# Optimization experiments

Measured on AMD Instinct MI355X. Metric: run time of the kernel, lower is better.

## Reference

```python
import jax, jax.numpy as jnp
import numpy as np

DIM = 192
H = W = 56
WS = 7
SS = 3
NH = 6
HIDDEN = int(DIM * 4.0)
B = 32


def layer_norm(x, g, b, eps=1e-5):
    mu = jnp.mean(x, axis=-1, keepdims=True)
    var = jnp.var(x, axis=-1, keepdims=True)
    return (x - mu) * jax.lax.rsqrt(var + eps) * g + b


def window_partition(x, ws):
    # x: [B, H, W, C] -> [B*nW, ws*ws, C]
    Bb, Hh, Ww, C = x.shape
    x = x.reshape(Bb, Hh // ws, ws, Ww // ws, ws, C)
    x = x.transpose(0, 1, 3, 2, 4, 5)
    return x.reshape(-1, ws * ws, C)


def window_reverse(win, ws, Hh, Ww):
    C = win.shape[-1]
    Bb = win.shape[0] // ((Hh // ws) * (Ww // ws))
    x = win.reshape(Bb, Hh // ws, Ww // ws, ws, ws, C)
    x = x.transpose(0, 1, 3, 2, 4, 5)
    return x.reshape(Bb, Hh, Ww, C)


def setup_inputs() -> dict:
    key = jax.random.key(0)
    ks = jax.random.split(key, 14)
    s = 0.02
    return {
        "x": jax.random.normal(ks[0], (B, H * W, DIM), jnp.float32),
        "qkv_w": jax.random.normal(ks[1], (DIM, 3 * DIM), jnp.float32) * s,
        "qkv_b": jnp.zeros((3 * DIM,), jnp.float32),
        "proj_w": jax.random.normal(ks[2], (DIM, DIM), jnp.float32) * s,
        "proj_b": jnp.zeros((DIM,), jnp.float32),
        "g1": jnp.ones((DIM,), jnp.float32),
        "be1": jnp.zeros((DIM,), jnp.float32),
        "g2": jnp.ones((DIM,), jnp.float32),
        "be2": jnp.zeros((DIM,), jnp.float32),
        "w1": jax.random.normal(ks[3], (DIM, HIDDEN), jnp.float32) * s,
        "b1": jnp.zeros((HIDDEN,), jnp.float32),
        "w2": jax.random.normal(ks[4], (HIDDEN, DIM), jnp.float32) * s,
        "b2": jnp.zeros((DIM,), jnp.float32),
    }


def reference(x, qkv_w, qkv_b, proj_w, proj_b, g1, be1, g2, be2, w1, b1, w2, b2):
    Bb, L, C = x.shape
    hd = C // NH
    scale = hd ** (-0.5)
    x4 = x.reshape(Bb, H, W, C)
    # cyclic shift
    shifted = jnp.roll(x4, shift=(-SS, -SS), axis=(1, 2))
    win = window_partition(shifted, WS)              # [B_, N, C]
    B_, N, _ = win.shape
    xn = layer_norm(win, g1, be1)
    qkv = xn @ qkv_w + qkv_b                          # [B_, N, 3C]
    qkv = qkv.reshape(B_, N, 3, NH, hd).transpose(2, 0, 3, 1, 4)
    q, k, v = qkv[0], qkv[1], qkv[2]                  # [B_, NH, N, hd]
    attn = jnp.einsum('bhnd,bhmd->bhnm', q, k) * scale
    attn = jax.nn.softmax(attn, axis=-1)
    out = jnp.einsum('bhnm,bhmd->bhnd', attn, v)
    out = out.transpose(0, 2, 1, 3).reshape(B_, N, C)
    out = out @ proj_w + proj_b
    x4 = window_reverse(out, WS, H, W)
    x4 = jnp.roll(x4, shift=(SS, SS), axis=(1, 2))
    x = x4.reshape(Bb, H * W, C)
    # MLP with residual
    xn2 = layer_norm(x, g2, be2)
    h = jax.nn.gelu(xn2 @ w1 + b1, approximate=False)
    return x + (h @ w2 + b2)
```

## Files before the change

kernel.cpp:

```cpp
#include <hip/hip_runtime.h>

typedef unsigned short u16;
typedef unsigned int   u32;
typedef __attribute__((ext_vector_type(8))) short bf16x8;
typedef __attribute__((ext_vector_type(4))) float f32x4;

#define DIMC   192
#define HH     56
#define WSZ    7
#define SSH    3
#define NTOK   49
#define NWIN_T 2048
#define HIDDEN 768
#define LTOT   3136

#define LDA    200
#define LDSS   68
#define LDPU   136
#define LDVT   72

#define OFF_QKV 0
#define OFF_PW  110592
#define OFF_W1  147456
#define OFF_W2  294912
#define WS_ELEMS 442368
#define WS_BYTES (WS_ELEMS * 2)
#define XATTN_BYTES ((size_t)NWIN_T * NTOK * DIMC * 2)

#define MFMA(a,b,c) __builtin_amdgcn_mfma_f32_16x16x32_bf16((a),(b),(c),0,0,0)

__device__ __forceinline__ float bf2f(u16 u) {
    union { u32 i; float f; } v; v.i = ((u32)u) << 16; return v.f;
}
__device__ __forceinline__ u16 f2bf(float f) {
    union { float ff; u32 i; } v; v.ff = f;
    u32 x = v.i;
    return (u16)((x + 0x7FFFu + ((x >> 16) & 1u)) >> 16);
}

__global__ void cvt_weights(const float* __restrict__ qkv_w,
                            const float* __restrict__ proj_w,
                            const float* __restrict__ w1,
                            const float* __restrict__ w2,
                            u16* __restrict__ ws)
{
    const int idx = blockIdx.x * blockDim.x + threadIdx.x;
    const int stride = gridDim.x * blockDim.x;
    for (int i = idx; i < 110592; i += stride) {
        int k = i / 576, n = i - k * 576;
        ws[OFF_QKV + n * 192 + k] = f2bf(qkv_w[i]);
    }
    for (int i = idx; i < 36864; i += stride) {
        int k = i / 192, n = i - k * 192;
        ws[OFF_PW + n * 192 + k] = f2bf(proj_w[i]);
    }
    for (int i = idx; i < 147456; i += stride) {
        int k = i / 768, n = i - k * 768;
        ws[OFF_W1 + n * 192 + k] = f2bf(w1[i]);
    }
    for (int i = idx; i < 147456; i += stride) {
        int k = i / 192, n = i - k * 192;
        ws[OFF_W2 + n * 768 + k] = f2bf(w2[i]);
    }
}

__device__ __forceinline__ void ln1_gather(
    const float* __restrict__ x, const float* __restrict__ g1,
    const float* __restrict__ be1, u16* __restrict__ s_A,
    int b, int wi, int wj, int wv, int lane)
{
    for (int t = wv; t < 64; t += 4) {
        if (t < NTOK) {
            const int pi = t / 7, pj = t - pi * 7;
            const int si = (wi * WSZ + pi + SSH) % HH;
            const int sj = (wj * WSZ + pj + SSH) % HH;
            const float* src = x + ((size_t)b * LTOT + si * HH + sj) * DIMC;
            float v0 = src[lane], v1 = src[lane + 64], v2 = src[lane + 128];
            float s  = v0 + v1 + v2;
            float s2 = v0 * v0 + v1 * v1 + v2 * v2;
#pragma unroll
            for (int off = 32; off > 0; off >>= 1) {
                s  += __shfl_xor(s,  off);
                s2 += __shfl_xor(s2, off);
            }
            const float mu   = s * (1.f / 192.f);
            const float rstd = rsqrtf(s2 * (1.f / 192.f) - mu * mu + 1e-5f);
            s_A[t*LDA + lane      ] = f2bf((v0-mu)*rstd*g1[lane]     + be1[lane]);
            s_A[t*LDA + lane + 64 ] = f2bf((v1-mu)*rstd*g1[lane+64]  + be1[lane+64]);
            s_A[t*LDA + lane + 128] = f2bf((v2-mu)*rstd*g1[lane+128] + be1[lane+128]);
        } else {
            s_A[t*LDA + lane] = 0; s_A[t*LDA + lane + 64] = 0; s_A[t*LDA + lane + 128] = 0;
        }
    }
}

__device__ __forceinline__ void attn_all(
    u16* __restrict__ s_A, u16* __restrict__ s_Q,
    float* __restrict__ Sf, u16* __restrict__ PU, u16* __restrict__ Vt,
    const u16* __restrict__ Wqkvt, const float* __restrict__ qkv_b,
    int tid, int wv, int ar, int ak, int rg0)
{
    const float scale = 0.1767766952966369f;
    f32x4 o[12];

    bf16x8 ax[4][6];
#pragma unroll
    for (int mt = 0; mt < 4; mt++)
#pragma unroll
        for (int kk = 0; kk < 6; kk++)
            ax[mt][kk] = *(const bf16x8*)&s_A[(mt*16 + ar)*LDA + kk*32 + ak];

#pragma unroll
    for (int G = 0; G < 3; G++) {
#pragma unroll
        for (int tl = 0; tl < 3; tl++) {
            const int tt = wv*3 + tl;
            const int section = tt >> 2, idxq = tt & 3;
            const int gcol = section*192 + G*64 + idxq*16 + ar;
            const int lcol = section*64 + idxq*16 + ar;
            const float bias = qkv_b[gcol];
            const u16* wc = Wqkvt + (size_t)gcol * 192;
            f32x4 acc[4];
#pragma unroll
            for (int mt = 0; mt < 4; mt++) acc[mt] = 0;
#pragma unroll
            for (int kk = 0; kk < 6; kk++) {
                bf16x8 bh = *(const bf16x8*)&wc[kk*32 + ak];
#pragma unroll
                for (int mt = 0; mt < 4; mt++)
                    acc[mt] = MFMA(ax[mt][kk], bh, acc[mt]);
            }
#pragma unroll
            for (int mt = 0; mt < 4; mt++)
#pragma unroll
                for (int rg = 0; rg < 4; rg++)
                    s_Q[(mt*16 + rg0 + rg)*LDA + lcol] = f2bf(acc[mt][rg] + bias);
        }
        __syncthreads();

#pragma unroll
        for (int HL = 0; HL < 2; HL++) {
            {
                bf16x8 bk = *(const bf16x8*)&s_Q[(wv*16 + ar)*LDA + 64 + HL*32 + ak];
#pragma unroll
                for (int mt = 0; mt < 4; mt++) {
                    bf16x8 aq = *(const bf16x8*)&s_Q[(mt*16 + ar)*LDA + HL*32 + ak];
                    f32x4 sa; sa = 0;
                    sa = MFMA(aq, bk, sa);
#pragma unroll
                    for (int rg = 0; rg < 4; rg++)
                        Sf[(mt*16 + rg0 + rg)*LDSS + wv*16 + ar] = sa[rg] * scale;
                }
            }
            __syncthreads();
            {
                const int row = tid >> 2, sub = tid & 3;
                if (row < NTOK) {
                    float e[16]; float m = -1e30f;
#pragma unroll
                    for (int i = 0; i < 16; i++) {
                        const int j = sub + 4*i;
                        e[i] = (j < NTOK) ? Sf[row*LDSS + j] : -1e30f;
                        m = fmaxf(m, e[i]);
                    }
                    m = fmaxf(m, __shfl_xor(m, 1));
                    m = fmaxf(m, __shfl_xor(m, 2));
                    float sum = 0.f;
#pragma unroll
                    for (int i = 0; i < 16; i++) { e[i] = __expf(e[i] - m); sum += e[i]; }
                    sum += __shfl_xor(sum, 1);
                    sum += __shfl_xor(sum, 2);
                    const float inv = 1.f / sum;
#pragma unroll
                    for (int i = 0; i < 16; i++) {
                        const int j = sub + 4*i;
                        const float p = e[i] * inv;
                        const u16 hb = f2bf(p);
                        PU[row*LDPU + j] = hb;
                        PU[row*LDPU + 64 + j] = f2bf(p - bf2f(hb));
                    }
                }
                for (int i2 = tid; i2 < 2048; i2 += 256) {
                    const int d = i2 & 31, j = i2 >> 5;
                    Vt[d*LDVT + j] = (j < NTOK) ? s_Q[j*LDA + 128 + HL*32 + d] : (u16)0;
                }
            }
            __syncthreads();
            {
                const int dcol = (wv & 1)*16 + ar;
                const int mtb = (wv >> 1) << 1;
#pragma unroll
                for (int mi = 0; mi < 2; mi++) {
                    f32x4 accv; accv = 0;
#pragma unroll
                    for (int kk = 0; kk < 2; kk++) {
                        bf16x8 ph = *(const bf16x8*)&PU[((mtb+mi)*16 + ar)*LDPU + kk*32 + ak];
                        bf16x8 pl = *(const bf16x8*)&PU[((mtb+mi)*16 + ar)*LDPU + 64 + kk*32 + ak];
                        bf16x8 bv = *(const bf16x8*)&Vt[dcol*LDVT + kk*32 + ak];
                        accv = MFMA(ph, bv, accv);
                        accv = MFMA(pl, bv, accv);
                    }
                    o[(G*2 + HL)*2 + mi] = accv;
                }
            }
            __syncthreads();
        }
    }

    {
        const int mtb = (wv >> 1) << 1;
        const int cbase = (wv & 1)*16 + ar;
#pragma unroll
        for (int hp = 0; hp < 6; hp++) {
            const int col = hp*32 + cbase;
#pragma unroll
            for (int mi = 0; mi < 2; mi++)
#pragma unroll
                for (int rg = 0; rg < 4; rg++)
                    s_A[((mtb+mi)*16 + rg0 + rg)*LDA + col] = f2bf(o[hp*2 + mi][rg]);
        }
    }
    __syncthreads();
}

__global__ __launch_bounds__(256, 2)
void swin_attn(const float* __restrict__ x,
               const float* __restrict__ qkv_b, const float* __restrict__ proj_b,
               const float* __restrict__ g1, const float* __restrict__ be1,
               const u16* __restrict__ wsw, u16* __restrict__ xattn)
{
    __shared__ __align__(16) u16 s_A[64 * LDA];
    __shared__ __align__(16) u16 s_Q[64 * LDA];
    __shared__ __align__(16) u16 s_R3[64 * LDPU + 32 * LDVT];

    float* const Sf = (float*)s_R3;
    u16*  const PU  = s_R3;
    u16*  const Vt  = s_R3 + 64 * LDPU;

    const int wid = blockIdx.x;
    const int b  = wid >> 6;
    const int wi = (wid >> 3) & 7;
    const int wj = wid & 7;
    const int tid  = threadIdx.x;
    const int wv   = tid >> 6;
    const int lane = tid & 63;
    const int ar   = lane & 15;
    const int ak   = (lane >> 4) << 3;
    const int rg0  = (lane >> 4) << 2;

    ln1_gather(x, g1, be1, s_A, b, wi, wj, wv, lane);
    __syncthreads();

    attn_all(s_A, s_Q, Sf, PU, Vt, wsw + OFF_QKV, qkv_b, tid, wv, ar, ak, rg0);

    {
        const u16* Wpt = wsw + OFF_PW;
        bf16x8 ao[4][6];
#pragma unroll
        for (int mt = 0; mt < 4; mt++)
#pragma unroll
            for (int kk = 0; kk < 6; kk++)
                ao[mt][kk] = *(const bf16x8*)&s_A[(mt*16 + ar)*LDA + kk*32 + ak];
#pragma unroll
        for (int ntl = 0; ntl < 3; ntl++) {
            const int col = (wv*3 + ntl)*16 + ar;
            const float bias = proj_b[col];
            const u16* wc = Wpt + (size_t)col * 192;
            f32x4 acc[4];
#pragma unroll
            for (int mt = 0; mt < 4; mt++) acc[mt] = 0;
#pragma unroll
            for (int kk = 0; kk < 6; kk++) {
                bf16x8 bh = *(const bf16x8*)&wc[kk*32 + ak];
#pragma unroll
                for (int mt = 0; mt < 4; mt++)
                    acc[mt] = MFMA(ao[mt][kk], bh, acc[mt]);
            }
#pragma unroll
            for (int mt = 0; mt < 4; mt++)
#pragma unroll
                for (int rg = 0; rg < 4; rg++) {
                    const int row = mt*16 + rg0 + rg;
                    if (row < NTOK)
                        xattn[((size_t)wid * NTOK + row) * DIMC + col] =
                            f2bf(acc[mt][rg] + bias);
                }
        }
    }
}

__global__ __launch_bounds__(256, 3)
void swin_mlp(const u16* __restrict__ xattn,
              const float* __restrict__ g2, const float* __restrict__ be2,
              const float* __restrict__ b1f, const float* __restrict__ b2f,
              const u16* __restrict__ wsw, float* __restrict__ out)
{
    __shared__ __align__(16) u16 s_X[64 * LDA];
    __shared__ __align__(16) u16 s_H[64 * LDA];

    const int tid  = threadIdx.x;
    const int wv   = tid >> 6;
    const int lane = tid & 63;
    const int ar   = lane & 15;
    const int ak   = (lane >> 4) << 3;
    const int rg0  = (lane >> 4) << 2;
    const int base = blockIdx.x * 64;
    const u16* W1t = wsw + OFF_W1;
    const u16* W2t = wsw + OFF_W2;

    for (int t = wv; t < 64; t += 4) {
        const u16* src = xattn + (size_t)(base + t) * DIMC;
        float v0 = bf2f(src[lane]);
        float v1 = bf2f(src[lane + 64]);
        float v2 = bf2f(src[lane + 128]);
        float s  = v0 + v1 + v2;
        float s2 = v0*v0 + v1*v1 + v2*v2;
#pragma unroll
        for (int off = 32; off > 0; off >>= 1) {
            s  += __shfl_xor(s,  off);
            s2 += __shfl_xor(s2, off);
        }
        const float mu   = s * (1.f / 192.f);
        const float rstd = rsqrtf(s2 * (1.f / 192.f) - mu * mu + 1e-5f);
        s_X[t*LDA + lane      ] = f2bf((v0-mu)*rstd*g2[lane]     + be2[lane]);
        s_X[t*LDA + lane + 64 ] = f2bf((v1-mu)*rstd*g2[lane+64]  + be2[lane+64]);
        s_X[t*LDA + lane + 128] = f2bf((v2-mu)*rstd*g2[lane+128] + be2[lane+128]);
    }
    __syncthreads();

    f32x4 accO[3][4];
#pragma unroll
    for (int i = 0; i < 3; i++)
#pragma unroll
        for (int m = 0; m < 4; m++) accO[i][m] = 0;

    for (int cc = 0; cc < 4; cc++) {
        {
            f32x4 acc1[3][4];
#pragma unroll
            for (int i = 0; i < 3; i++)
#pragma unroll
                for (int m = 0; m < 4; m++) acc1[i][m] = 0;
#pragma unroll
            for (int kk = 0; kk < 6; kk++) {
                bf16x8 a4[4];
#pragma unroll
                for (int mt = 0; mt < 4; mt++)
                    a4[mt] = *(const bf16x8*)&s_X[(mt*16 + ar)*LDA + kk*32 + ak];
#pragma unroll
                for (int ntl = 0; ntl < 3; ntl++) {
                    const int ngl = cc*192 + (wv*3 + ntl)*16 + ar;
                    bf16x8 w = *(const bf16x8*)&W1t[(size_t)ngl * 192 + kk*32 + ak];
#pragma unroll
                    for (int mt = 0; mt < 4; mt++)
                        acc1[ntl][mt] = MFMA(a4[mt], w, acc1[ntl][mt]);
                }
            }
#pragma unroll
            for (int ntl = 0; ntl < 3; ntl++) {
                const int ncol = (wv*3 + ntl)*16 + ar;
                const float bias = b1f[cc*192 + ncol];
#pragma unroll
                for (int mt = 0; mt < 4; mt++)
#pragma unroll
                    for (int rg = 0; rg < 4; rg++) {
                        const float z = acc1[ntl][mt][rg] + bias;
                        const float ge = 0.5f * z * (1.f + erff(z * 0.70710678118654752f));
                        s_H[(mt*16 + rg0 + rg)*LDA + ncol] = f2bf(ge);
                    }
            }
        }
        __syncthreads();
        {
#pragma unroll
            for (int kk = 0; kk < 6; kk++) {
                bf16x8 a4[4];
#pragma unroll
                for (int mt = 0; mt < 4; mt++)
                    a4[mt] = *(const bf16x8*)&s_H[(mt*16 + ar)*LDA + kk*32 + ak];
#pragma unroll
                for (int ntl = 0; ntl < 3; ntl++) {
                    const int col = (wv*3 + ntl)*16 + ar;
                    bf16x8 w = *(const bf16x8*)&W2t[(size_t)col * 768 + cc*192 + kk*32 + ak];
#pragma unroll
                    for (int mt = 0; mt < 4; mt++)
                        accO[ntl][mt] = MFMA(a4[mt], w, accO[ntl][mt]);
                }
            }
        }
        __syncthreads();
    }

#pragma unroll
    for (int ntl = 0; ntl < 3; ntl++) {
        const int col = (wv*3 + ntl)*16 + ar;
        const float bias = b2f[col];
#pragma unroll
        for (int mt = 0; mt < 4; mt++)
#pragma unroll
            for (int rg = 0; rg < 4; rg++) {
                const int grow = base + mt*16 + rg0 + rg;
                const int w = grow / 49, t = grow - w * 49;
                const int bb = w >> 6, wi = (w >> 3) & 7, wj = w & 7;
                const int pi = t / 7, pj = t - pi * 7;
                const int di = (wi * WSZ + pi + SSH) % HH;
                const int dj = (wj * WSZ + pj + SSH) % HH;
                out[((size_t)bb * LTOT + di * HH + dj) * DIMC + col] =
                    accO[ntl][mt][rg] + bias + bf2f(xattn[(size_t)grow * DIMC + col]);
            }
    }
}

__global__ __launch_bounds__(256, 2)
void swin_mono(const float* __restrict__ x,
               const float* __restrict__ qkv_b, const float* __restrict__ proj_b,
               const float* __restrict__ g1, const float* __restrict__ be1,
               const float* __restrict__ g2, const float* __restrict__ be2,
               const float* __restrict__ b1f, const float* __restrict__ b2f,
               const u16* __restrict__ wsw, float* __restrict__ out)
{
    __shared__ __align__(16) u16 s_A[64 * LDA];
    __shared__ __align__(16) u16 s_Q[64 * LDA];
    __shared__ __align__(16) u16 s_R3[64 * LDA];

    float* const Sf  = (float*)s_R3;
    u16*  const PU   = s_R3;
    u16*  const Vt   = s_R3 + 64 * LDPU;
    u16*  const s_H  = s_R3;
    u16*  const s_XW = s_Q;

    const int wid = blockIdx.x;
    const int b  = wid >> 6;
    const int wi = (wid >> 3) & 7;
    const int wj = wid & 7;
    const int tid  = threadIdx.x;
    const int wv   = tid >> 6;
    const int lane = tid & 63;
    const int ar   = lane & 15;
    const int ak   = (lane >> 4) << 3;
    const int rg0  = (lane >> 4) << 2;

    const u16* Wpt = wsw + OFF_PW;
    const u16* W1t = wsw + OFF_W1;
    const u16* W2t = wsw + OFF_W2;

    ln1_gather(x, g1, be1, s_A, b, wi, wj, wv, lane);
    __syncthreads();

    attn_all(s_A, s_Q, Sf, PU, Vt, wsw + OFF_QKV, qkv_b, tid, wv, ar, ak, rg0);

    {
        bf16x8 ao[4][6];
#pragma unroll
        for (int mt = 0; mt < 4; mt++)
#pragma unroll
            for (int kk = 0; kk < 6; kk++)
                ao[mt][kk] = *(const bf16x8*)&s_A[(mt*16 + ar)*LDA + kk*32 + ak];
#pragma unroll
        for (int ntl = 0; ntl < 3; ntl++) {
            const int col = (wv*3 + ntl)*16 + ar;
            const float bias = proj_b[col];
            const u16* wc = Wpt + (size_t)col * 192;
            f32x4 acc[4];
#pragma unroll
            for (int mt = 0; mt < 4; mt++) acc[mt] = 0;
#pragma unroll
            for (int kk = 0; kk < 6; kk++) {
                bf16x8 bh = *(const bf16x8*)&wc[kk*32 + ak];
#pragma unroll
                for (int mt = 0; mt < 4; mt++)
                    acc[mt] = MFMA(ao[mt][kk], bh, acc[mt]);
            }
#pragma unroll
            for (int mt = 0; mt < 4; mt++)
#pragma unroll
                for (int rg = 0; rg < 4; rg++)
                    s_XW[(mt*16 + rg0 + rg)*LDA + col] = f2bf(acc[mt][rg] + bias);
        }
    }
    __syncthreads();

    for (int t = wv; t < NTOK; t += 4) {
        float v0 = bf2f(s_XW[t*LDA + lane      ]);
        float v1 = bf2f(s_XW[t*LDA + lane + 64 ]);
        float v2 = bf2f(s_XW[t*LDA + lane + 128]);
        float s  = v0 + v1 + v2;
        float s2 = v0*v0 + v1*v1 + v2*v2;
#pragma unroll
        for (int off = 32; off > 0; off >>= 1) {
            s  += __shfl_xor(s,  off);
            s2 += __shfl_xor(s2, off);
        }
        const float mu   = s * (1.f / 192.f);
        const float rstd = rsqrtf(s2 * (1.f / 192.f) - mu * mu + 1e-5f);
        s_A[t*LDA + lane      ] = f2bf((v0-mu)*rstd*g2[lane]     + be2[lane]);
        s_A[t*LDA + lane + 64 ] = f2bf((v1-mu)*rstd*g2[lane+64]  + be2[lane+64]);
        s_A[t*LDA + lane + 128] = f2bf((v2-mu)*rstd*g2[lane+128] + be2[lane+128]);
    }
    __syncthreads();

    f32x4 accO[3][4];
#pragma unroll
    for (int i = 0; i < 3; i++)
#pragma unroll
        for (int m = 0; m < 4; m++) accO[i][m] = 0;

    for (int cc = 0; cc < 4; cc++) {
        {
            f32x4 acc1[3][4];
#pragma unroll
            for (int i = 0; i < 3; i++)
#pragma unroll
                for (int m = 0; m < 4; m++) acc1[i][m] = 0;
#pragma unroll
            for (int kk = 0; kk < 6; kk++) {
                bf16x8 a4[4];
#pragma unroll
                for (int mt = 0; mt < 4; mt++)
                    a4[mt] = *(const bf16x8*)&s_A[(mt*16 + ar)*LDA + kk*32 + ak];
#pragma unroll
                for (int ntl = 0; ntl < 3; ntl++) {
                    const int ngl = cc*192 + (wv*3 + ntl)*16 + ar;
                    bf16x8 w = *(const bf16x8*)&W1t[(size_t)ngl * 192 + kk*32 + ak];
#pragma unroll
                    for (int mt = 0; mt < 4; mt++)
                        acc1[ntl][mt] = MFMA(a4[mt], w, acc1[ntl][mt]);
                }
            }
#pragma unroll
            for (int ntl = 0; ntl < 3; ntl++) {
                const int ncol = (wv*3 + ntl)*16 + ar;
                const float bias = b1f[cc*192 + ncol];
#pragma unroll
                for (int mt = 0; mt < 4; mt++)
#pragma unroll
                    for (int rg = 0; rg < 4; rg++) {
                        const float z = acc1[ntl][mt][rg] + bias;
                        const float ge = 0.5f * z * (1.f + erff(z * 0.70710678118654752f));
                        s_H[(mt*16 + rg0 + rg)*LDA + ncol] = f2bf(ge);
                    }
            }
        }
        __syncthreads();
        {
#pragma unroll
            for (int kk = 0; kk < 6; kk++) {
                bf16x8 a4[4];
#pragma unroll
                for (int mt = 0; mt < 4; mt++)
                    a4[mt] = *(const bf16x8*)&s_H[(mt*16 + ar)*LDA + kk*32 + ak];
#pragma unroll
                for (int ntl = 0; ntl < 3; ntl++) {
                    const int col = (wv*3 + ntl)*16 + ar;
                    bf16x8 w = *(const bf16x8*)&W2t[(size_t)col * 768 + cc*192 + kk*32 + ak];
#pragma unroll
                    for (int mt = 0; mt < 4; mt++)
                        accO[ntl][mt] = MFMA(a4[mt], w, accO[ntl][mt]);
                }
            }
        }
        __syncthreads();
    }

#pragma unroll
    for (int ntl = 0; ntl < 3; ntl++) {
        const int col = (wv*3 + ntl)*16 + ar;
        const float bias = b2f[col];
#pragma unroll
        for (int mt = 0; mt < 4; mt++)
#pragma unroll
            for (int rg = 0; rg < 4; rg++) {
                const int row = mt*16 + rg0 + rg;
                if (row < NTOK) {
                    const int pi = row / 7, pj = row - pi * 7;
                    const int di = (wi * WSZ + pi + SSH) % HH;
                    const int dj = (wj * WSZ + pj + SSH) % HH;
                    out[((size_t)b * LTOT + di * HH + dj) * DIMC + col] =
                        accO[ntl][mt][rg] + bias + bf2f(s_XW[row*LDA + col]);
                }
            }
    }
}

extern "C" void kernel_launch(void* const* d_in, const int* in_sizes, int n_in,
                              void* d_out, int out_size, void* d_ws, size_t ws_size,
                              hipStream_t stream)
{
    const float* x      = (const float*)d_in[0];
    const float* qkv_w  = (const float*)d_in[1];
    const float* qkv_b  = (const float*)d_in[2];
    const float* proj_w = (const float*)d_in[3];
    const float* proj_b = (const float*)d_in[4];
    const float* g1     = (const float*)d_in[5];
    const float* be1    = (const float*)d_in[6];
    const float* g2     = (const float*)d_in[7];
    const float* be2    = (const float*)d_in[8];
    const float* w1     = (const float*)d_in[9];
    const float* b1     = (const float*)d_in[10];
    const float* w2     = (const float*)d_in[11];
    const float* b2     = (const float*)d_in[12];
    float* out = (float*)d_out;

    cvt_weights<<<256, 256, 0, stream>>>(qkv_w, proj_w, w1, w2, (u16*)d_ws);

    if (ws_size >= (size_t)WS_BYTES + XATTN_BYTES) {
        u16* xattn = (u16*)d_ws + WS_ELEMS;
        swin_attn<<<NWIN_T, 256, 0, stream>>>(x, qkv_b, proj_b, g1, be1,
                                              (const u16*)d_ws, xattn);
        swin_mlp<<<NTOK * NWIN_T / 64, 256, 0, stream>>>(xattn, g2, be2, b1, b2,
                                                         (const u16*)d_ws, out);
    } else {
        swin_mono<<<NWIN_T, 256, 0, stream>>>(x, qkv_b, proj_b, g1, be1, g2, be2,
                                              b1, b2, (const u16*)d_ws, out);
    }
}
```

Baseline: 349.8 us.

## Split fused MLP kernel into separate GEMM1+GELU and GEMM2+residual kernels

Replaces the single fused MLP kernel with two kernels: one does LayerNorm, the first GEMM and GELU over 64-row by 192-column chunks, writing the hidden activation to a bf16 workspace buffer. The second reads that buffer and performs the second GEMM, bias, residual and un-shift scatter. This gives four times more blocks for the first GEMM and lighter per-block register and LDS use, aiming at higher occupancy. In exchange it adds a large global round trip for the hidden tensor, recomputes LayerNorm per column chunk, and reads A operands for the second GEMM straight from global memory without LDS staging. The new path runs only if the workspace is large enough.

Result: slower. 451.7 us (+29.1%).

```diff
diff --git a/kernel.cpp b/kernel.cpp
--- a/kernel.cpp
+++ b/kernel.cpp
@@ -13,6 +13,7 @@
 #define NWIN_T 2048
 #define HIDDEN 768
 #define LTOT   3136
+#define NTOKENS 100352
 
 #define LDA    200
 #define LDSS   68
@@ -25,7 +26,10 @@
 #define OFF_W2  294912
 #define WS_ELEMS 442368
 #define WS_BYTES (WS_ELEMS * 2)
-#define XATTN_BYTES ((size_t)NWIN_T * NTOK * DIMC * 2)
+#define XATTN_ELEMS ((size_t)NWIN_T * NTOK * DIMC)
+#define XATTN_BYTES (XATTN_ELEMS * 2)
+#define H_ELEMS ((size_t)NTOKENS * HIDDEN)
+#define H_BYTES (H_ELEMS * 2)
 
 #define MFMA(a,b,c) __builtin_amdgcn_mfma_f32_16x16x32_bf16((a),(b),(c),0,0,0)
 
@@ -286,6 +290,138 @@
                             f2bf(acc[mt][rg] + bias);
                 }
         }
+    }
+}
+
+__global__ __launch_bounds__(256, 4)
+void mlp1_gelu(const u16* __restrict__ xattn,
+               const float* __restrict__ g2, const float* __restrict__ be2,
+               const float* __restrict__ b1f,
+               const u16* __restrict__ wsw, u16* __restrict__ hbuf)
+{
+    __shared__ __align__(16) u16 s_X[64 * LDA];
+
+    const int bid = blockIdx.x;
+    const int rb = bid >> 2, cchunk = bid & 3;
+    const size_t base = (size_t)rb * 64;
+    const int tid  = threadIdx.x;
+    const int wv   = tid >> 6;
+    const int lane = tid & 63;
+    const int ar   = lane & 15;
+    const int ak   = (lane >> 4) << 3;
+    const int rg0  = (lane >> 4) << 2;
+    const u16* W1t = wsw + OFF_W1;
+
+    for (int t = wv; t < 64; t += 4) {
+        const u16* src = xattn + (base + t) * DIMC;
+        float v0 = bf2f(src[lane]);
+        float v1 = bf2f(src[lane + 64]);
+        float v2 = bf2f(src[lane + 128]);
+        float s  = v0 + v1 + v2;
+        float s2 = v0*v0 + v1*v1 + v2*v2;
+#pragma unroll
+        for (int off = 32; off > 0; off >>= 1) {
+            s  += __shfl_xor(s,  off);
+            s2 += __shfl_xor(s2, off);
+        }
+        const float mu   = s * (1.f / 192.f);
+        const float rstd = rsqrtf(s2 * (1.f / 192.f) - mu * mu + 1e-5f);
+        s_X[t*LDA + lane      ] = f2bf((v0-mu)*rstd*g2[lane]     + be2[lane]);
+        s_X[t*LDA + lane + 64 ] = f2bf((v1-mu)*rstd*g2[lane+64]  + be2[lane+64]);
+        s_X[t*LDA + lane + 128] = f2bf((v2-mu)*rstd*g2[lane+128] + be2[lane+128]);
+    }
+    __syncthreads();
+
+    f32x4 acc1[3][4];
+#pragma unroll
+    for (int i = 0; i < 3; i++)
+#pragma unroll
+        for (int m = 0; m < 4; m++) acc1[i][m] = 0;
+
+#pragma unroll
+    for (int kk = 0; kk < 6; kk++) {
+        bf16x8 a4[4];
+#pragma unroll
+        for (int mt = 0; mt < 4; mt++)
+            a4[mt] = *(const bf16x8*)&s_X[(mt*16 + ar)*LDA + kk*32 + ak];
+#pragma unroll
+        for (int ntl = 0; ntl < 3; ntl++) {
+            const int ngl = cchunk*192 + (wv*3 + ntl)*16 + ar;
+            bf16x8 w = *(const bf16x8*)&W1t[(size_t)ngl * 192 + kk*32 + ak];
+#pragma unroll
+            for (int mt = 0; mt < 4; mt++)
+                acc1[ntl][mt] = MFMA(a4[mt], w, acc1[ntl][mt]);
+        }
+    }
+#pragma unroll
+    for (int ntl = 0; ntl < 3; ntl++) {
+        const int ngl = cchunk*192 + (wv*3 + ntl)*16 + ar;
+        const float bias = b1f[ngl];
+#pragma unroll
+        for (int mt = 0; mt < 4; mt++)
+#pragma unroll
+            for (int rg = 0; rg < 4; rg++) {
+                const float z = acc1[ntl][mt][rg] + bias;
+                const float ge = 0.5f * z * (1.f + erff(z * 0.70710678118654752f));
+                hbuf[(base + mt*16 + rg0 + rg) * HIDDEN + ngl] = f2bf(ge);
+            }
+    }
+}
+
+__global__ __launch_bounds__(256, 4)
+void mlp2_resid(const u16* __restrict__ hbuf, const u16* __restrict__ xattn,
+                const float* __restrict__ b2f,
+                const u16* __restrict__ wsw, float* __restrict__ out)
+{
+    const int rb = blockIdx.x;
+    const size_t base = (size_t)rb * 64;
+    const int tid  = threadIdx.x;
+    const int wv   = tid >> 6;
+    const int lane = tid & 63;
+    const int ar   = lane & 15;
+    const int ak   = (lane >> 4) << 3;
+    const int rg0  = (lane >> 4) << 2;
+    const u16* W2t = wsw + OFF_W2;
+
+    f32x4 accO[3][4];
+#pragma unroll
+    for (int i = 0; i < 3; i++)
+#pragma unroll
+        for (int m = 0; m < 4; m++) accO[i][m] = 0;
+
+#pragma unroll 4
+    for (int kk = 0; kk < 24; kk++) {
+        bf16x8 a4[4];
+#pragma unroll
+        for (int mt = 0; mt < 4; mt++)
+            a4[mt] = *(const bf16x8*)&hbuf[(base + mt*16 + ar) * HIDDEN + kk*32 + ak];
+#pragma unroll
+        for (int ntl = 0; ntl < 3; ntl++) {
+            const int col = (wv*3 + ntl)*16 + ar;
+            bf16x8 w = *(const bf16x8*)&W2t[(size_t)col * HIDDEN + kk*32 + ak];
+#pragma unroll
+            for (int mt = 0; mt < 4; mt++)
+                accO[ntl][mt] = MFMA(a4[mt], w, accO[ntl][mt]);
+        }
+    }
+
+#pragma unroll
+    for (int ntl = 0; ntl < 3; ntl++) {
+        const int col = (wv*3 + ntl)*16 + ar;
+        const float bias = b2f[col];
+#pragma unroll
+        for (int mt = 0; mt < 4; mt++)
+#pragma unroll
+            for (int rg = 0; rg < 4; rg++) {
+                const size_t grow = base + mt*16 + rg0 + rg;
+                const int w = (int)(grow / 49), t = (int)(grow - (size_t)w * 49);
+                const int bb = w >> 6, wi = (w >> 3) & 7, wj = w & 7;
+                const int pi = t / 7, pj = t - pi * 7;
+                const int di = (wi * WSZ + pi + SSH) % HH;
+                const int dj = (wj * WSZ + pj + SSH) % HH;
+                out[((size_t)bb * LTOT + di * HH + dj) * DIMC + col] =
+                    accO[ntl][mt][rg] + bias + bf2f(xattn[grow * DIMC + col]);
+            }
     }
 }
 
@@ -603,12 +739,21 @@
 
     cvt_weights<<<256, 256, 0, stream>>>(qkv_w, proj_w, w1, w2, (u16*)d_ws);
 
-    if (ws_size >= (size_t)WS_BYTES + XATTN_BYTES) {
+    if (ws_size >= (size_t)WS_BYTES + XATTN_BYTES + H_BYTES) {
+        u16* xattn = (u16*)d_ws + WS_ELEMS;
+        u16* hbuf  = (u16*)d_ws + WS_ELEMS + XATTN_ELEMS;
+        swin_attn<<<NWIN_T, 256, 0, stream>>>(x, qkv_b, proj_b, g1, be1,
+                                              (const u16*)d_ws, xattn);
+        mlp1_gelu<<<(NTOKENS/64)*4, 256, 0, stream>>>(xattn, g2, be2, b1,
+                                                      (const u16*)d_ws, hbuf);
+        mlp2_resid<<<NTOKENS/64, 256, 0, stream>>>(hbuf, xattn, b2,
+                                                   (const u16*)d_ws, out);
+    } else if (ws_size >= (size_t)WS_BYTES + XATTN_BYTES) {
         u16* xattn = (u16*)d_ws + WS_ELEMS;
         swin_attn<<<NWIN_T, 256, 0, stream>>>(x, qkv_b, proj_b, g1, be1,
                                               (const u16*)d_ws, xattn);
-        swin_mlp<<<NTOK * NWIN_T / 64, 256, 0, stream>>>(xattn, g2, be2, b1, b2,
-                                                         (const u16*)d_ws, out);
+        swin_mlp<<<NTOKENS/64, 256, 0, stream>>>(xattn, g2, be2, b1, b2,
+                                                 (const u16*)d_ws, out);
     } else {
         swin_mono<<<NWIN_T, 256, 0, stream>>>(x, qkv_b, proj_b, g1, be1, g2, be2,
                                               b1, b2, (const u16*)d_ws, out);
```

## Software-pipeline MLP chunks with double-buffered hidden tile in LDS

Applied to the files above, without the earlier changes.

Restructures the MLP kernel so the second GEMM for hidden chunk cc is interleaved with the first GEMM plus GELU for chunk cc+1. The hidden activations are double-buffered in shared memory, which removes one barrier per chunk and gives the scheduler independent MFMA streams to overlap. In exchange, LDS use grows by one extra 64x200 buffer, register pressure rises, and launch bounds drop from 3 to 2 blocks per CU, so occupancy falls.

Result: slower. 400.0 us (+14.4%).

```diff
diff --git a/kernel.cpp b/kernel.cpp
--- a/kernel.cpp
+++ b/kernel.cpp
@@ -13,6 +13,7 @@
 #define NWIN_T 2048
 #define HIDDEN 768
 #define LTOT   3136
+#define NTOKENS 100352
 
 #define LDA    200
 #define LDSS   68
@@ -25,7 +26,8 @@
 #define OFF_W2  294912
 #define WS_ELEMS 442368
 #define WS_BYTES (WS_ELEMS * 2)
-#define XATTN_BYTES ((size_t)NWIN_T * NTOK * DIMC * 2)
+#define XATTN_ELEMS ((size_t)NWIN_T * NTOK * DIMC)
+#define XATTN_BYTES (XATTN_ELEMS * 2)
 
 #define MFMA(a,b,c) __builtin_amdgcn_mfma_f32_16x16x32_bf16((a),(b),(c),0,0,0)
 
@@ -289,14 +291,14 @@
     }
 }
 
-__global__ __launch_bounds__(256, 3)
+__global__ __launch_bounds__(256, 2)
 void swin_mlp(const u16* __restrict__ xattn,
               const float* __restrict__ g2, const float* __restrict__ be2,
               const float* __restrict__ b1f, const float* __restrict__ b2f,
               const u16* __restrict__ wsw, float* __restrict__ out)
 {
     __shared__ __align__(16) u16 s_X[64 * LDA];
-    __shared__ __align__(16) u16 s_H[64 * LDA];
+    __shared__ __align__(16) u16 s_H[2][64 * LDA];
 
     const int tid  = threadIdx.x;
     const int wv   = tid >> 6;
@@ -328,14 +330,54 @@
     }
     __syncthreads();
 
+    {
+        f32x4 acc1[3][4];
+#pragma unroll
+        for (int i = 0; i < 3; i++)
+#pragma unroll
+            for (int m = 0; m < 4; m++) acc1[i][m] = 0;
+#pragma unroll
+        for (int kk = 0; kk < 6; kk++) {
+            bf16x8 a4[4];
+#pragma unroll
+            for (int mt = 0; mt < 4; mt++)
+                a4[mt] = *(const bf16x8*)&s_X[(mt*16 + ar)*LDA + kk*32 + ak];
+#pragma unroll
+            for (int ntl = 0; ntl < 3; ntl++) {
+                const int ngl = (wv*3 + ntl)*16 + ar;
+                bf16x8 w = *(const bf16x8*)&W1t[(size_t)ngl * 192 + kk*32 + ak];
+#pragma unroll
+                for (int mt = 0; mt < 4; mt++)
+                    acc1[ntl][mt] = MFMA(a4[mt], w, acc1[ntl][mt]);
+            }
+        }
+#pragma unroll
+        for (int ntl = 0; ntl < 3; ntl++) {
+            const int ncol = (wv*3 + ntl)*16 + ar;
+            const float bias = b1f[ncol];
+#pragma unroll
+            for (int mt = 0; mt < 4; mt++)
+#pragma unroll
+                for (int rg = 0; rg < 4; rg++) {
+                    const float z = acc1[ntl][mt][rg] + bias;
+                    const float ge = 0.5f * z * (1.f + erff(z * 0.70710678118654752f));
+                    s_H[0][(mt*16 + rg0 + rg)*LDA + ncol] = f2bf(ge);
+                }
+        }
+    }
+    __syncthreads();
+
     f32x4 accO[3][4];
 #pragma unroll
     for (int i = 0; i < 3; i++)
 #pragma unroll
         for (int m = 0; m < 4; m++) accO[i][m] = 0;
 
+#pragma unroll
     for (int cc = 0; cc < 4; cc++) {
-        {
+        const u16* hcur = &s_H[cc & 1][0];
+        if (cc < 3) {
+            u16* hnxt = &s_H[(cc + 1) & 1][0];
             f32x4 acc1[3][4];
 #pragma unroll
             for (int i = 0; i < 3; i++)
@@ -343,48 +385,53 @@
                 for (int m = 0; m < 4; m++) acc1[i][m] = 0;
 #pragma unroll
             for (int kk = 0; kk < 6; kk++) {
-                bf16x8 a4[4];
-#pragma unroll
-                for (int mt = 0; mt < 4; mt++)
-                    a4[mt] = *(const bf16x8*)&s_X[(mt*16 + ar)*LDA + kk*32 + ak];
+                bf16x8 a4h[4], a4x[4];
+#pragma unroll
+                for (int mt = 0; mt < 4; mt++) {
+                    a4h[mt] = *(const bf16x8*)&hcur[(mt*16 + ar)*LDA + kk*32 + ak];
+                    a4x[mt] = *(const bf16x8*)&s_X[(mt*16 + ar)*LDA + kk*32 + ak];
+                }
 #pragma unroll
                 for (int ntl = 0; ntl < 3; ntl++) {
-                    const int ngl = cc*192 + (wv*3 + ntl)*16 + ar;
-                    bf16x8 w = *(const bf16x8*)&W1t[(size_t)ngl * 192 + kk*32 + ak];
+                    const int col = (wv*3 + ntl)*16 + ar;
+                    bf16x8 w2 = *(const bf16x8*)&W2t[(size_t)col * 768 + cc*192 + kk*32 + ak];
 #pragma unroll
                     for (int mt = 0; mt < 4; mt++)
-                        acc1[ntl][mt] = MFMA(a4[mt], w, acc1[ntl][mt]);
+                        accO[ntl][mt] = MFMA(a4h[mt], w2, accO[ntl][mt]);
+                    const int ngl = (cc + 1)*192 + col;
+                    bf16x8 w1 = *(const bf16x8*)&W1t[(size_t)ngl * 192 + kk*32 + ak];
+#pragma unroll
+                    for (int mt = 0; mt < 4; mt++)
+                        acc1[ntl][mt] = MFMA(a4x[mt], w1, acc1[ntl][mt]);
                 }
             }
 #pragma unroll
             for (int ntl = 0; ntl < 3; ntl++) {
                 const int ncol = (wv*3 + ntl)*16 + ar;
-                const float bias = b1f[cc*192 + ncol];
+                const float bias = b1f[(cc + 1)*192 + ncol];
 #pragma unroll
                 for (int mt = 0; mt < 4; mt++)
 #pragma unroll
                     for (int rg = 0; rg < 4; rg++) {
                         const float z = acc1[ntl][mt][rg] + bias;
                         const float ge = 0.5f * z * (1.f + erff(z * 0.70710678118654752f));
-                        s_H[(mt*16 + rg0 + rg)*LDA + ncol] = f2bf(ge);
+                        hnxt[(mt*16 + rg0 + rg)*LDA + ncol] = f2bf(ge);
                     }
             }
-        }
-        __syncthreads();
-        {
+        } else {
 #pragma unroll
             for (int kk = 0; kk < 6; kk++) {
-                bf16x8 a4[4];
-#pragma unroll
-                for (int mt = 0; mt < 4; mt++)
-                    a4[mt] = *(const bf16x8*)&s_H[(mt*16 + ar)*LDA + kk*32 + ak];
+                bf16x8 a4h[4];
+#pragma unroll
+                for (int mt = 0; mt < 4; mt++)
+                    a4h[mt] = *(const bf16x8*)&hcur[(mt*16 + ar)*LDA + kk*32 + ak];
 #pragma unroll
                 for (int ntl = 0; ntl < 3; ntl++) {
                     const int col = (wv*3 + ntl)*16 + ar;
-                    bf16x8 w = *(const bf16x8*)&W2t[(size_t)col * 768 + cc*192 + kk*32 + ak];
+                    bf16x8 w2 = *(const bf16x8*)&W2t[(size_t)col * 768 + cc*192 + kk*32 + ak];
 #pragma unroll
                     for (int mt = 0; mt < 4; mt++)
-                        accO[ntl][mt] = MFMA(a4[mt], w, accO[ntl][mt]);
+                        accO[ntl][mt] = MFMA(a4h[mt], w2, accO[ntl][mt]);
                 }
             }
         }
@@ -607,8 +654,8 @@
         u16* xattn = (u16*)d_ws + WS_ELEMS;
         swin_attn<<<NWIN_T, 256, 0, stream>>>(x, qkv_b, proj_b, g1, be1,
                                               (const u16*)d_ws, xattn);
-        swin_mlp<<<NTOK * NWIN_T / 64, 256, 0, stream>>>(xattn, g2, be2, b1, b2,
-                                                         (const u16*)d_ws, out);
+        swin_mlp<<<NTOKENS/64, 256, 0, stream>>>(xattn, g2, be2, b1, b2,
+                                                 (const u16*)d_ws, out);
     } else {
         swin_mono<<<NWIN_T, 256, 0, stream>>>(x, qkv_b, proj_b, g1, be1, g2, be2,
                                               b1, b2, (const u16*)d_ws, out);
```

## Alias attention scratch onto s_A and use polynomial erf for GELU

Applied to the files above, without the earlier changes.

Removes the separate s_R3 shared buffer in the attention kernel by aliasing score, probability and V-transpose scratch onto s_A, cutting LDS per block so three blocks can be resident (launch bounds raised to 3). Replaces erff in the MLP GELU with an Abramowitz-Stegun polynomial approximation using a fast reciprocal and exp. The aliasing relies on s_A being dead during the softmax/PV phase, and the restrict qualifiers are dropped accordingly. The GELU approximation adds small error, which bf16 rounding largely masks.

New measurement: 385.3 us. +10.1%, slower.

```diff
diff --git a/kernel.cpp b/kernel.cpp
--- a/kernel.cpp
+++ b/kernel.cpp
@@ -13,6 +13,7 @@
 #define NWIN_T 2048
 #define HIDDEN 768
 #define LTOT   3136
+#define NTOKENS 100352
 
 #define LDA    200
 #define LDSS   68
@@ -25,7 +26,8 @@
 #define OFF_W2  294912
 #define WS_ELEMS 442368
 #define WS_BYTES (WS_ELEMS * 2)
-#define XATTN_BYTES ((size_t)NWIN_T * NTOK * DIMC * 2)
+#define XATTN_ELEMS ((size_t)NWIN_T * NTOK * DIMC)
+#define XATTN_BYTES (XATTN_ELEMS * 2)
 
 #define MFMA(a,b,c) __builtin_amdgcn_mfma_f32_16x16x32_bf16((a),(b),(c),0,0,0)
 
@@ -36,6 +38,19 @@
     union { float ff; u32 i; } v; v.ff = f;
     u32 x = v.i;
     return (u16)((x + 0x7FFFu + ((x >> 16) & 1u)) >> 16);
+}
+
+__device__ __forceinline__ float gelu_fast(float z) {
+    const float x = fabsf(z) * 0.70710678118654752f;
+    const float t = __frcp_rn(fmaf(0.3275911f, x, 1.f));
+    float p = fmaf(1.061405429f, t, -1.453152027f);
+    p = fmaf(p, t, 1.421413741f);
+    p = fmaf(p, t, -0.284496736f);
+    p = fmaf(p, t, 0.254829592f);
+    const float e = __expf(-x * x);
+    float erfv = 1.f - p * t * e;
+    erfv = copysignf(erfv, z);
+    return 0.5f * z * (1.f + erfv);
 }
 
 __global__ void cvt_weights(const float* __restrict__ qkv_w,
@@ -96,7 +111,7 @@
 
 __device__ __forceinline__ void attn_all(
     u16* __restrict__ s_A, u16* __restrict__ s_Q,
-    float* __restrict__ Sf, u16* __restrict__ PU, u16* __restrict__ Vt,
+    float* Sf, u16* PU, u16* Vt,
     const u16* __restrict__ Wqkvt, const float* __restrict__ qkv_b,
     int tid, int wv, int ar, int ak, int rg0)
 {
@@ -223,7 +238,7 @@
     __syncthreads();
 }
 
-__global__ __launch_bounds__(256, 2)
+__global__ __launch_bounds__(256, 3)
 void swin_attn(const float* __restrict__ x,
                const float* __restrict__ qkv_b, const float* __restrict__ proj_b,
                const float* __restrict__ g1, const float* __restrict__ be1,
@@ -231,11 +246,10 @@
 {
     __shared__ __align__(16) u16 s_A[64 * LDA];
     __shared__ __align__(16) u16 s_Q[64 * LDA];
-    __shared__ __align__(16) u16 s_R3[64 * LDPU + 32 * LDVT];
-
-    float* const Sf = (float*)s_R3;
-    u16*  const PU  = s_R3;
-    u16*  const Vt  = s_R3 + 64 * LDPU;
+
+    float* const Sf = (float*)s_A;
+    u16*  const PU  = s_A;
+    u16*  const Vt  = s_A + 64 * LDPU;
 
     const int wid = blockIdx.x;
     const int b  = wid >> 6;
@@ -365,8 +379,7 @@
 #pragma unroll
                     for (int rg = 0; rg < 4; rg++) {
                         const float z = acc1[ntl][mt][rg] + bias;
-                        const float ge = 0.5f * z * (1.f + erff(z * 0.70710678118654752f));
-                        s_H[(mt*16 + rg0 + rg)*LDA + ncol] = f2bf(ge);
+                        s_H[(mt*16 + rg0 + rg)*LDA + ncol] = f2bf(gelu_fast(z));
                     }
             }
         }
@@ -536,8 +549,7 @@
 #pragma unroll
                     for (int rg = 0; rg < 4; rg++) {
                         const float z = acc1[ntl][mt][rg] + bias;
-                        const float ge = 0.5f * z * (1.f + erff(z * 0.70710678118654752f));
-                        s_H[(mt*16 + rg0 + rg)*LDA + ncol] = f2bf(ge);
+                        s_H[(mt*16 + rg0 + rg)*LDA + ncol] = f2bf(gelu_fast(z));
                     }
             }
         }
@@ -607,8 +619,8 @@
         u16* xattn = (u16*)d_ws + WS_ELEMS;
         swin_attn<<<NWIN_T, 256, 0, stream>>>(x, qkv_b, proj_b, g1, be1,
                                               (const u16*)d_ws, xattn);
-        swin_mlp<<<NTOK * NWIN_T / 64, 256, 0, stream>>>(xattn, g2, be2, b1, b2,
-                                                         (const u16*)d_ws, out);
+        swin_mlp<<<NTOKENS/64, 256, 0, stream>>>(xattn, g2, be2, b1, b2,
+                                                 (const u16*)d_ws, out);
     } else {
         swin_mono<<<NWIN_T, 256, 0, stream>>>(x, qkv_b, proj_b, g1, be1, g2, be2,
                                               b1, b2, (const u16*)d_ws, out);
```
